# Performance work log

Hardware: AMD Instinct MI355X
Metric: run time of the kernel (lower is better)

The kernel has to match this reference:

```python
import jax, jax.numpy as jnp
import numpy as np

S, B, D, F, E, K = 1024, 2, 512, 2048, 8, 2


def setup_inputs() -> dict:
    key = jax.random.key(0)
    ks = jax.random.split(key, 12)
    s = lambda *sh: 1.0 / np.sqrt(sh[0])
    inp = {
        "x": jax.random.normal(ks[0], (S, B, D), dtype=jnp.float32),
        # gate: nn.Linear(d_model, n_experts)
        "Wg": jax.random.normal(ks[1], (D, E), dtype=jnp.float32) * s(D),
        "bg": jnp.zeros((E,), dtype=jnp.float32),
        # routed experts: stacked FFN params (E copies of expert)
        "W1": jax.random.normal(ks[2], (E, D, F), dtype=jnp.float32) * s(D),
        "b1": jnp.zeros((E, F), dtype=jnp.float32),
        "W2": jax.random.normal(ks[3], (E, F, D), dtype=jnp.float32) * s(F),
        "b2": jnp.zeros((E, D), dtype=jnp.float32),
        # shared expert (single FFN)
        "Ws1": jax.random.normal(ks[4], (D, F), dtype=jnp.float32) * s(D),
        "bs1": jnp.zeros((F,), dtype=jnp.float32),
        "Ws2": jax.random.normal(ks[5], (F, D), dtype=jnp.float32) * s(F),
        "bs2": jnp.zeros((D,), dtype=jnp.float32),
    }
    return inp


def reference(x, Wg, bg, W1, b1, W2, b2, Ws1, bs1, Ws2, bs2):
    # gate_logits: (S, B, E)
    gate_logits = jnp.einsum("sbd,de->sbe", x, Wg) + bg
    # top-k per token (eval mode: k = n_experts_per_token, t = 1.0)
    weights, selected = jax.lax.top_k(gate_logits, K)  # (S,B,K)
    weights = jax.nn.softmax(weights.astype(jnp.float32), axis=-1)
    # combine weights per expert: (S,B,E)
    onehot = jax.nn.one_hot(selected, E, dtype=weights.dtype)  # (S,B,K,E)
    comb = jnp.einsum("sbk,sbke->sbe", weights, onehot)
    # routed experts computed densely, combined with per-token routing weight
    h = jax.nn.relu(jnp.einsum("sbd,edf->sbef", x, W1) + b1)  # (S,B,E,F)
    y = jnp.einsum("sbef,efd->sbed", h, W2) + b2              # (S,B,E,D)
    out = jnp.einsum("sbe,sbed->sbd", comb, y)
    # shared expert, scaled by 1/k
    hs = jax.nn.relu(jnp.einsum("sbd,df->sbf", x, Ws1) + bs1)
    shared = jnp.einsum("sbf,fd->sbd", hs, Ws2) + bs2
    out = out + (1.0 / K) * shared
    return out
```

## Files before the change

kernel.cpp:

```cpp
#include <hip/hip_runtime.h>
#include <hip/hip_bf16.h>
#include <stdint.h>

#define TT 2048
#define DD 512
#define FF 2048
#define EE 8

typedef unsigned short u16;
typedef __attribute__((ext_vector_type(8))) unsigned short ushort8v;
typedef __attribute__((ext_vector_type(8))) short short8;
typedef __attribute__((ext_vector_type(4))) float float4v;

__device__ __forceinline__ u16 f2bf(float f) {
    unsigned u = __float_as_uint(f);
    u += 0x7FFF + ((u >> 16) & 1);
    return (u16)(u >> 16);
}

__device__ __forceinline__ void gl_lds16(const u16* g, u16* l) {
    __builtin_amdgcn_global_load_lds(
        (const __attribute__((address_space(1))) unsigned int*)g,
        (__attribute__((address_space(3))) unsigned int*)l, 16, 0, 0);
}

#define WS_HB   0ull
#define WS_XG   (WS_HB + 6144ull*2048*2)
#define WS_WT1  (WS_XG + 2048ull*512*2)
#define WS_ME   (WS_WT1 + 9ull*2048*512*2)
#define WS_MW   (WS_ME + 16384)
#define WS_RT   (WS_MW + 16384)
#define WS_WROW (WS_RT + 16384)
#define WS_RTG  (WS_WROW + 16384)
#define WS_WT2  (WS_RTG + 128)
#define WS_NEED (WS_WT2 + 9ull*2048*512*2)

__device__ __forceinline__ void conv_unit(int j, const float* __restrict__ srcE,
                                          const float* __restrict__ srcS,
                                          u16* __restrict__ dst,
                                          int R, int C, int shC, u16* Ls) {
    int mid = j >> 8, t2 = j & 255;
    int tr = t2 >> shC, tc = t2 & ((1 << shC) - 1);
    int r0 = tr * 64, c0 = tc * 64;
    const float* src = (mid < 8) ? srcE + (size_t)mid * R * C : srcS;
    u16* dstm = dst + (size_t)mid * R * C;
    int t = threadIdx.x;
#pragma unroll
    for (int i = 0; i < 4; ++i) {
        int rr = (t >> 4) + i * 16;
        int cc = (t & 15) * 4;
        float4v v = *(const float4v*)(src + (size_t)(r0 + rr) * C + c0 + cc);
#pragma unroll
        for (int jx = 0; jx < 4; ++jx) Ls[(cc + jx) * 72 + rr] = f2bf(v[jx]);
    }
    __syncthreads();
#pragma unroll
    for (int jj = 0; jj < 2; ++jj) {
        int slot = t + jj * 256;
        int cc = slot >> 3, r8 = (slot & 7) * 8;
        ushort8v o = *(const ushort8v*)&Ls[cc * 72 + r8];
        *(ushort8v*)(dstm + (size_t)(c0 + cc) * R + r0 + r8) = o;
    }
}

__device__ __forceinline__ void gate_wave(int t, int lane,
                                          const float* __restrict__ x,
                                          const float* __restrict__ Wg,
                                          const float* __restrict__ bg,
                                          int* __restrict__ metaE,
                                          float* __restrict__ metaW,
                                          u16* __restrict__ xg) {
    const float* xp = x + (size_t)t * DD + lane * 8;
    float4v x0 = *(const float4v*)xp;
    float4v x1 = *(const float4v*)(xp + 4);
    float xf[8] = {x0[0], x0[1], x0[2], x0[3], x1[0], x1[1], x1[2], x1[3]};
    float acc[EE] = {0.f, 0.f, 0.f, 0.f, 0.f, 0.f, 0.f, 0.f};
#pragma unroll
    for (int g = 0; g < 8; ++g) {
        const float* wp = Wg + (size_t)(lane * 8 + g) * EE;
        float4v w0 = *(const float4v*)wp;
        float4v w1 = *(const float4v*)(wp + 4);
        acc[0] += xf[g] * w0[0]; acc[1] += xf[g] * w0[1];
        acc[2] += xf[g] * w0[2]; acc[3] += xf[g] * w0[3];
        acc[4] += xf[g] * w1[0]; acc[5] += xf[g] * w1[1];
        acc[6] += xf[g] * w1[2]; acc[7] += xf[g] * w1[3];
    }
#pragma unroll
    for (int off = 1; off < 64; off <<= 1) {
#pragma unroll
        for (int e = 0; e < EE; ++e) acc[e] += __shfl_xor(acc[e], off, 64);
    }
    ushort8v xv;
#pragma unroll
    for (int jx = 0; jx < 4; ++jx) xv[jx] = f2bf(x0[jx]);
#pragma unroll
    for (int jx = 0; jx < 4; ++jx) xv[4 + jx] = f2bf(x1[jx]);
    *(ushort8v*)(xg + (size_t)t * DD + lane * 8) = xv;
    if (lane == 0) {
#pragma unroll
        for (int e = 0; e < EE; ++e) acc[e] += bg[e];
        int e0 = 0; float l0 = acc[0];
#pragma unroll
        for (int e = 1; e < EE; ++e) if (acc[e] > l0) { l0 = acc[e]; e0 = e; }
        int e1 = -1; float l1 = -3.4e38f;
#pragma unroll
        for (int e = 0; e < EE; ++e)
            if (e != e0 && acc[e] > l1) { l1 = acc[e]; e1 = e; }
        float ex = __expf(l1 - l0);
        float w0 = 1.f / (1.f + ex);
        metaE[2 * t] = e0; metaE[2 * t + 1] = e1;
        metaW[2 * t] = w0; metaW[2 * t + 1] = 1.f - w0;
    }
}

__global__ __launch_bounds__(256) void fused1_k(
    const float* __restrict__ x, const float* __restrict__ Wg,
    const float* __restrict__ bg,
    const float* __restrict__ W1, const float* __restrict__ Ws1,
    const float* __restrict__ W2, const float* __restrict__ Ws2,
    float* __restrict__ out, u16* __restrict__ xg,
    u16* __restrict__ Wt1, u16* __restrict__ Wt2,
    int* __restrict__ metaE, float* __restrict__ metaW, int nconv) {
    __shared__ __align__(16) u16 Ls[64 * 72];
    int b = blockIdx.x, tid = threadIdx.x;
    if (b < nconv) {
        if (b < 2304) conv_unit(b, W1, Ws1, Wt1, DD, FF, 5, Ls);
        else          conv_unit(b - 2304, W2, Ws2, Wt2, FF, DD, 3, Ls);
    } else if (b < nconv + 512) {
        int gb = b - nconv;
        gate_wave(gb * 4 + (tid >> 6), tid & 63, x, Wg, bg, metaE, metaW, xg);
    } else {
        int zb = b - nconv - 512;
        float* op = out + (size_t)zb * 8192;
#pragma unroll
        for (int it = 0; it < 8; ++it)
            *(float4v*)(op + it * 1024 + tid * 4) = (float4v){0.f, 0.f, 0.f, 0.f};
    }
}

__global__ __launch_bounds__(256) void conv2_k(const float* __restrict__ W2,
                                               const float* __restrict__ Ws2,
                                               u16* __restrict__ Wt2) {
    __shared__ __align__(16) u16 Ls[64 * 72];
    conv_unit(blockIdx.x, W2, Ws2, Wt2, FF, DD, 3, Ls);
}

__global__ __launch_bounds__(256) void rank_k(const int* __restrict__ metaE,
                                              const float* __restrict__ metaW,
                                              int* __restrict__ routing,
                                              int* __restrict__ rtok,
                                              float* __restrict__ wrow) {
    __shared__ __align__(16) char smem[16384];
    u16* er      = (u16*)smem;
    int* segCnt  = (int*)(smem + 8192);
    int* segBase = (int*)(smem + 10240);
    int* expTot  = (int*)(smem + 12288);
    int tid = threadIdx.x, wv = tid >> 6, lane = tid & 63;
    unsigned long long below = (lane == 0) ? 0ull : ((~0ull) >> (64 - lane));
    for (int s = wv * 16; s < wv * 16 + 16; ++s) {
        int entry = s * 64 + lane;
        int e = metaE[entry];
        int rk = 0;
#pragma unroll
        for (int ee = 0; ee < 8; ++ee) {
            unsigned long long m = __ballot(e == ee);
            if (e == ee) rk = __popcll(m & below);
            if (lane == ee) segCnt[s * 8 + ee] = __popcll(m);
        }
        er[entry] = (u16)(e | (rk << 4));
    }
    __syncthreads();
    if (tid < 8) {
        int s = 0;
        for (int g = 0; g < 64; ++g) { segBase[g * 8 + tid] = s; s += segCnt[g * 8 + tid]; }
        expTot[tid] = s;
    }
    __syncthreads();
    if (tid == 0) {
        int s = 0;
        for (int e = 0; e < 8; ++e) { int c = expTot[e]; expTot[8 + e] = s; s += c; }
    }
    __syncthreads();
    if (tid < 8) { routing[tid] = expTot[8 + tid]; routing[8 + tid] = expTot[tid]; }
    for (int i = 0; i < 16; ++i) {
        int entry = tid + i * 256;
        int v = er[entry];
        int e = v & 15, rk = v >> 4;
        int row = expTot[8 + e] + segBase[(entry >> 6) * 8 + e] + rk;
        rtok[row] = entry >> 1;
        wrow[row] = metaW[entry];
    }
}

__global__ __launch_bounds__(256) void gemmA_k(
    const u16* __restrict__ xg, const u16* __restrict__ Wt1,
    const float* __restrict__ b1, const float* __restrict__ bs1,
    const int* __restrict__ routing, const int* __restrict__ rtok,
    u16* __restrict__ hbuf) {
    __shared__ __align__(16) u16 As[64 * 128];
    __shared__ __align__(16) u16 Bs[128 * 128];
    const int* offs = routing; const int* cnt = routing + 8;
    int j = blockIdx.x, tid = threadIdx.x;
    int rt, ct, Mloc, hRowBase, rowBase; bool routed;
    const u16* Bsrc; const float* bias;
    if (j < 512) {
        rt = j >> 4; ct = j & 15; Mloc = 64; rowBase = rt * 64;
        Bsrc = Wt1 + (size_t)8 * FF * DD; bias = bs1;
        hRowBase = 4096 + rt * 64; routed = false;
    } else {
        int jr = j - 512; int e = jr & 7; int rc = jr >> 3;
        rt = rc >> 4; ct = rc & 15;
        int M = cnt[e]; if (rt * 64 >= M) return;
        Mloc = M - rt * 64; if (Mloc > 64) Mloc = 64;
        rowBase = offs[e] + rt * 64;
        Bsrc = Wt1 + (size_t)e * FF * DD; bias = b1 + e * FF;
        hRowBase = rowBase; routed = true;
    }
    int n0 = ct * 128;
    int lane = tid & 63, w = tid >> 6, ln = lane & 15, quad = lane >> 4;
    int l4 = lane >> 4;
    int cpre = lane & 15;
    const u16* Ap[4];
#pragma unroll
    for (int i = 0; i < 4; ++i) {
        int g = i * 4 + w;
        int r = g * 4 + l4;
        int c = cpre ^ (r & 15);
        int tok;
        if (routed) {
            int br = rowBase + r; if (br > 4095) br = 4095;
            tok = rtok[br];
        } else tok = rowBase + r;
        Ap[i] = xg + (size_t)tok * DD + c * 8;
    }
    const u16* Bp[8];
#pragma unroll
    for (int i = 0; i < 8; ++i) {
        int g = i * 4 + w;
        int r = g * 4 + l4;
        int c = cpre ^ (r & 15);
        Bp[i] = Bsrc + (size_t)(n0 + r) * DD + c * 8;
    }
    float4v acc[2][4];
#pragma unroll
    for (int a = 0; a < 2; ++a)
#pragma unroll
        for (int b = 0; b < 4; ++b) acc[a][b] = (float4v){0.f, 0.f, 0.f, 0.f};
    for (int kt = 0; kt < 4; ++kt) {
        int k0 = kt * 128;
#pragma unroll
        for (int i = 0; i < 4; ++i)
            gl_lds16(Ap[i] + k0, &As[(i * 4 + w) * 512]);
#pragma unroll
        for (int i = 0; i < 8; ++i)
            gl_lds16(Bp[i] + k0, &Bs[(i * 4 + w) * 512]);
        __syncthreads();
#pragma unroll
        for (int s = 0; s < 4; ++s) {
            int slot = ((s * 4 + quad) ^ ln) * 8;
            short8 Af[2], Bf[4];
#pragma unroll
            for (int a = 0; a < 2; ++a)
                Af[a] = *(const short8*)&As[((w & 1) * 32 + a * 16 + ln) * 128 + slot];
#pragma unroll
            for (int b = 0; b < 4; ++b)
                Bf[b] = *(const short8*)&Bs[((w >> 1) * 64 + b * 16 + ln) * 128 + slot];
#pragma unroll
            for (int a = 0; a < 2; ++a)
#pragma unroll
                for (int b = 0; b < 4; ++b)
                    acc[a][b] = __builtin_amdgcn_mfma_f32_16x16x32_bf16(Af[a], Bf[b], acc[a][b], 0, 0, 0);
        }
        __syncthreads();
    }
#pragma unroll
    for (int b = 0; b < 4; ++b) {
        int n = n0 + (w >> 1) * 64 + b * 16 + ln;
        float bv = bias[n];
#pragma unroll
        for (int a = 0; a < 2; ++a) {
#pragma unroll
            for (int i = 0; i < 4; ++i) {
                int lr = (w & 1) * 32 + a * 16 + quad * 4 + i;
                if (lr < Mloc) {
                    float v = acc[a][b][i] + bv;
                    v = v > 0.f ? v : 0.f;
                    hbuf[(size_t)(hRowBase + lr) * FF + n] = f2bf(v);
                }
            }
        }
    }
}

__global__ __launch_bounds__(256) void gemmB_k(
    const u16* __restrict__ hbuf, const u16* __restrict__ Wt2,
    const float* __restrict__ b2, const float* __restrict__ bs2,
    const int* __restrict__ routing, const int* __restrict__ rtok,
    const float* __restrict__ wrow, float* __restrict__ out) {
    __shared__ __align__(16) u16 As[64 * 128];
    __shared__ __align__(16) u16 Bs[128 * 128];
    const int* offs = routing; const int* cnt = routing + 8;
    int j = blockIdx.x, tid = threadIdx.x;
    int rt, ct, ks, Mloc, aRowBase; bool sh;
    const u16* Bsrc; const float* bias;
    if (j < 256) {
        sh = true; rt = j >> 3; int sub = j & 7; ct = sub >> 1; ks = sub & 1;
        Mloc = 64; aRowBase = 4096 + rt * 64;
        Bsrc = Wt2 + (size_t)8 * DD * FF; bias = bs2;
    } else {
        sh = false; int jr = j - 256; int e = jr & 7; int rc = jr >> 3;
        rt = rc >> 3; ct = (rc >> 1) & 3; ks = rc & 1;
        int M = cnt[e]; if (rt * 64 >= M) return;
        Mloc = M - rt * 64; if (Mloc > 64) Mloc = 64;
        aRowBase = offs[e] + rt * 64;
        Bsrc = Wt2 + (size_t)e * DD * FF; bias = b2 + e * DD;
    }
    int n0 = ct * 128;
    int lane = tid & 63, w = tid >> 6, ln = lane & 15, quad = lane >> 4;
    int l4 = lane >> 4;
    int cpre = lane & 15;
    const u16* Ap[4];
#pragma unroll
    for (int i = 0; i < 4; ++i) {
        int g = i * 4 + w;
        int r = g * 4 + l4;
        int c = cpre ^ (r & 15);
        Ap[i] = hbuf + (size_t)(aRowBase + r) * FF + ks * 1024 + c * 8;
    }
    const u16* Bp[8];
#pragma unroll
    for (int i = 0; i < 8; ++i) {
        int g = i * 4 + w;
        int r = g * 4 + l4;
        int c = cpre ^ (r & 15);
        Bp[i] = Bsrc + (size_t)(n0 + r) * FF + ks * 1024 + c * 8;
    }
    float4v acc[2][4];
#pragma unroll
    for (int a = 0; a < 2; ++a)
#pragma unroll
        for (int b = 0; b < 4; ++b) acc[a][b] = (float4v){0.f, 0.f, 0.f, 0.f};
    for (int kt = 0; kt < 8; ++kt) {
        int k0 = kt * 128;
#pragma unroll
        for (int i = 0; i < 4; ++i)
            gl_lds16(Ap[i] + k0, &As[(i * 4 + w) * 512]);
#pragma unroll
        for (int i = 0; i < 8; ++i)
            gl_lds16(Bp[i] + k0, &Bs[(i * 4 + w) * 512]);
        __syncthreads();
#pragma unroll
        for (int s = 0; s < 4; ++s) {
            int slot = ((s * 4 + quad) ^ ln) * 8;
            short8 Af[2], Bf[4];
#pragma unroll
            for (int a = 0; a < 2; ++a)
                Af[a] = *(const short8*)&As[((w & 1) * 32 + a * 16 + ln) * 128 + slot];
#pragma unroll
            for (int b = 0; b < 4; ++b)
                Bf[b] = *(const short8*)&Bs[((w >> 1) * 64 + b * 16 + ln) * 128 + slot];
#pragma unroll
            for (int a = 0; a < 2; ++a)
#pragma unroll
                for (int b = 0; b < 4; ++b)
                    acc[a][b] = __builtin_amdgcn_mfma_f32_16x16x32_bf16(Af[a], Bf[b], acc[a][b], 0, 0, 0);
        }
        __syncthreads();
    }
    float bv[4];
#pragma unroll
    for (int b = 0; b < 4; ++b)
        bv[b] = (ks == 0) ? bias[n0 + (w >> 1) * 64 + b * 16 + ln] : 0.f;
#pragma unroll
    for (int a = 0; a < 2; ++a) {
#pragma unroll
        for (int i = 0; i < 4; ++i) {
            int lr = (w & 1) * 32 + a * 16 + quad * 4 + i;
            if (lr < Mloc) {
                int row = aRowBase + lr;
                int t; float wr;
                if (sh) { t = row - 4096; wr = 0.5f; }
                else    { t = rtok[row]; wr = wrow[row]; }
                float* op = out + (size_t)t * DD;
#pragma unroll
                for (int b = 0; b < 4; ++b) {
                    int n = n0 + (w >> 1) * 64 + b * 16 + ln;
                    atomicAdd(op + n, wr * (acc[a][b][i] + bv[b]));
                }
            }
        }
    }
}

extern "C" void kernel_launch(void* const* d_in, const int* in_sizes, int n_in,
                              void* d_out, int out_size, void* d_ws, size_t ws_size,
                              hipStream_t stream) {
    const float* x   = (const float*)d_in[0];
    const float* Wg  = (const float*)d_in[1];
    const float* bg  = (const float*)d_in[2];
    const float* W1  = (const float*)d_in[3];
    const float* b1  = (const float*)d_in[4];
    const float* W2  = (const float*)d_in[5];
    const float* b2  = (const float*)d_in[6];
    const float* Ws1 = (const float*)d_in[7];
    const float* bs1 = (const float*)d_in[8];
    const float* Ws2 = (const float*)d_in[9];
    const float* bs2 = (const float*)d_in[10];
    float* out = (float*)d_out;

    char* ws = (char*)d_ws;
    u16*   hbuf    = (u16*)(ws + WS_HB);
    u16*   xg      = (u16*)(ws + WS_XG);
    u16*   Wt1     = (u16*)(ws + WS_WT1);
    int*   metaE   = (int*)(ws + WS_ME);
    float* metaW   = (float*)(ws + WS_MW);
    int*   rtok    = (int*)(ws + WS_RT);
    float* wrow    = (float*)(ws + WS_WROW);
    int*   routing = (int*)(ws + WS_RTG);
    bool   big     = ws_size >= WS_NEED;
    u16*   Wt2     = big ? (u16*)(ws + WS_WT2) : Wt1;
    int    nconv   = big ? 4608 : 2304;

    fused1_k<<<nconv + 640, 256, 0, stream>>>(x, Wg, bg, W1, Ws1, W2, Ws2,
                                              out, xg, Wt1, Wt2, metaE, metaW, nconv);
    rank_k<<<1, 256, 0, stream>>>(metaE, metaW, routing, rtok, wrow);
    gemmA_k<<<8704, 256, 0, stream>>>(xg, Wt1, b1, bs1, routing, rtok, hbuf);
    if (!big) conv2_k<<<2304, 256, 0, stream>>>(W2, Ws2, Wt2);
    gemmB_k<<<4352, 256, 0, stream>>>(hbuf, Wt2, b2, bs2, routing, rtok, wrow, out);
}
```

Baseline: 215.9 us.

## Load MFMA operands directly from global memory, dropping LDS staging in expert GEMMs

Both expert GEMM kernels stop staging A and B tiles in shared memory through global_load_lds and barriers. Each wave now reads its MFMA fragments straight from global memory with fully unrolled K loops. This removes the LDS traffic and __syncthreads, but gives up on-chip data reuse: the B tile is loaded separately by the two waves that share it and the A tile by the two waves that share it, so global and L2 traffic roughly doubles. Each lane's 16-byte reads are also strided by row, so coalescing is poor.

New measurement: 324.4 us. +50.2%, slower.

```diff
diff --git a/kernel.cpp b/kernel.cpp
--- a/kernel.cpp
+++ b/kernel.cpp
@@ -197,8 +197,6 @@
     const float* __restrict__ b1, const float* __restrict__ bs1,
     const int* __restrict__ routing, const int* __restrict__ rtok,
     u16* __restrict__ hbuf) {
-    __shared__ __align__(16) u16 As[64 * 128];
-    __shared__ __align__(16) u16 Bs[128 * 128];
     const int* offs = routing; const int* cnt = routing + 8;
     int j = blockIdx.x, tid = threadIdx.x;
     int rt, ct, Mloc, hRowBase, rowBase; bool routed;
@@ -218,60 +216,40 @@
     }
     int n0 = ct * 128;
     int lane = tid & 63, w = tid >> 6, ln = lane & 15, quad = lane >> 4;
-    int l4 = lane >> 4;
-    int cpre = lane & 15;
-    const u16* Ap[4];
-#pragma unroll
-    for (int i = 0; i < 4; ++i) {
-        int g = i * 4 + w;
-        int r = g * 4 + l4;
-        int c = cpre ^ (r & 15);
+    const u16* Ap[2];
+#pragma unroll
+    for (int a = 0; a < 2; ++a) {
+        int r = (w & 1) * 32 + a * 16 + ln;
         int tok;
-        if (routed) {
-            int br = rowBase + r; if (br > 4095) br = 4095;
-            tok = rtok[br];
-        } else tok = rowBase + r;
-        Ap[i] = xg + (size_t)tok * DD + c * 8;
-    }
-    const u16* Bp[8];
-#pragma unroll
-    for (int i = 0; i < 8; ++i) {
-        int g = i * 4 + w;
-        int r = g * 4 + l4;
-        int c = cpre ^ (r & 15);
-        Bp[i] = Bsrc + (size_t)(n0 + r) * DD + c * 8;
-    }
+        if (routed) { int br = rowBase + r; if (br > 4095) br = 4095; tok = rtok[br]; }
+        else tok = rowBase + r;
+        Ap[a] = xg + (size_t)tok * DD + quad * 8;
+    }
+    const u16* Bp[4];
+#pragma unroll
+    for (int b = 0; b < 4; ++b)
+        Bp[b] = Bsrc + (size_t)(n0 + (w >> 1) * 64 + b * 16 + ln) * DD + quad * 8;
     float4v acc[2][4];
 #pragma unroll
     for (int a = 0; a < 2; ++a)
 #pragma unroll
         for (int b = 0; b < 4; ++b) acc[a][b] = (float4v){0.f, 0.f, 0.f, 0.f};
+#pragma unroll
     for (int kt = 0; kt < 4; ++kt) {
-        int k0 = kt * 128;
-#pragma unroll
-        for (int i = 0; i < 4; ++i)
-            gl_lds16(Ap[i] + k0, &As[(i * 4 + w) * 512]);
-#pragma unroll
-        for (int i = 0; i < 8; ++i)
-            gl_lds16(Bp[i] + k0, &Bs[(i * 4 + w) * 512]);
-        __syncthreads();
 #pragma unroll
         for (int s = 0; s < 4; ++s) {
-            int slot = ((s * 4 + quad) ^ ln) * 8;
+            int ko = kt * 128 + s * 32;
             short8 Af[2], Bf[4];
 #pragma unroll
-            for (int a = 0; a < 2; ++a)
-                Af[a] = *(const short8*)&As[((w & 1) * 32 + a * 16 + ln) * 128 + slot];
-#pragma unroll
-            for (int b = 0; b < 4; ++b)
-                Bf[b] = *(const short8*)&Bs[((w >> 1) * 64 + b * 16 + ln) * 128 + slot];
+            for (int a = 0; a < 2; ++a) Af[a] = *(const short8*)(Ap[a] + ko);
+#pragma unroll
+            for (int b = 0; b < 4; ++b) Bf[b] = *(const short8*)(Bp[b] + ko);
 #pragma unroll
             for (int a = 0; a < 2; ++a)
 #pragma unroll
                 for (int b = 0; b < 4; ++b)
                     acc[a][b] = __builtin_amdgcn_mfma_f32_16x16x32_bf16(Af[a], Bf[b], acc[a][b], 0, 0, 0);
         }
-        __syncthreads();
     }
 #pragma unroll
     for (int b = 0; b < 4; ++b) {
@@ -297,8 +275,6 @@
     const float* __restrict__ b2, const float* __restrict__ bs2,
     const int* __restrict__ routing, const int* __restrict__ rtok,
     const float* __restrict__ wrow, float* __restrict__ out) {
-    __shared__ __align__(16) u16 As[64 * 128];
-    __shared__ __align__(16) u16 Bs[128 * 128];
     const int* offs = routing; const int* cnt = routing + 8;
     int j = blockIdx.x, tid = threadIdx.x;
     int rt, ct, ks, Mloc, aRowBase; bool sh;
@@ -317,55 +293,37 @@
     }
     int n0 = ct * 128;
     int lane = tid & 63, w = tid >> 6, ln = lane & 15, quad = lane >> 4;
-    int l4 = lane >> 4;
-    int cpre = lane & 15;
-    const u16* Ap[4];
-#pragma unroll
-    for (int i = 0; i < 4; ++i) {
-        int g = i * 4 + w;
-        int r = g * 4 + l4;
-        int c = cpre ^ (r & 15);
-        Ap[i] = hbuf + (size_t)(aRowBase + r) * FF + ks * 1024 + c * 8;
-    }
-    const u16* Bp[8];
-#pragma unroll
-    for (int i = 0; i < 8; ++i) {
-        int g = i * 4 + w;
-        int r = g * 4 + l4;
-        int c = cpre ^ (r & 15);
-        Bp[i] = Bsrc + (size_t)(n0 + r) * FF + ks * 1024 + c * 8;
-    }
+    const u16* Ap[2];
+#pragma unroll
+    for (int a = 0; a < 2; ++a) {
+        int r = (w & 1) * 32 + a * 16 + ln;
+        Ap[a] = hbuf + (size_t)(aRowBase + r) * FF + ks * 1024 + quad * 8;
+    }
+    const u16* Bp[4];
+#pragma unroll
+    for (int b = 0; b < 4; ++b)
+        Bp[b] = Bsrc + (size_t)(n0 + (w >> 1) * 64 + b * 16 + ln) * FF + ks * 1024 + quad * 8;
     float4v acc[2][4];
 #pragma unroll
     for (int a = 0; a < 2; ++a)
 #pragma unroll
         for (int b = 0; b < 4; ++b) acc[a][b] = (float4v){0.f, 0.f, 0.f, 0.f};
+#pragma unroll
     for (int kt = 0; kt < 8; ++kt) {
-        int k0 = kt * 128;
-#pragma unroll
-        for (int i = 0; i < 4; ++i)
-            gl_lds16(Ap[i] + k0, &As[(i * 4 + w) * 512]);
-#pragma unroll
-        for (int i = 0; i < 8; ++i)
-            gl_lds16(Bp[i] + k0, &Bs[(i * 4 + w) * 512]);
-        __syncthreads();
 #pragma unroll
         for (int s = 0; s < 4; ++s) {
-            int slot = ((s * 4 + quad) ^ ln) * 8;
+            int ko = kt * 128 + s * 32;
             short8 Af[2], Bf[4];
 #pragma unroll
-            for (int a = 0; a < 2; ++a)
-                Af[a] = *(const short8*)&As[((w & 1) * 32 + a * 16 + ln) * 128 + slot];
-#pragma unroll
-            for (int b = 0; b < 4; ++b)
-                Bf[b] = *(const short8*)&Bs[((w >> 1) * 64 + b * 16 + ln) * 128 + slot];
+            for (int a = 0; a < 2; ++a) Af[a] = *(const short8*)(Ap[a] + ko);
+#pragma unroll
+            for (int b = 0; b < 4; ++b) Bf[b] = *(const short8*)(Bp[b] + ko);
 #pragma unroll
             for (int a = 0; a < 2; ++a)
 #pragma unroll
                 for (int b = 0; b < 4; ++b)
                     acc[a][b] = __builtin_amdgcn_mfma_f32_16x16x32_bf16(Af[a], Bf[b], acc[a][b], 0, 0, 0);
         }
-        __syncthreads();
     }
     float bv[4];
 #pragma unroll
```
